# Performance work log

Hardware: AMD Instinct MI355X
Metric: run time of the kernel (lower is better)

The kernel has to match this reference:

```python
import jax, jax.numpy as jnp
import numpy as np

B, C, P, T, H = 4, 256, 1024, 64, 8
D = C // H
SCALE = float(np.sqrt(D * T))


def setup_inputs() -> dict:
    key = jax.random.key(0)
    ks = jax.random.split(key, 7)
    s = 1.0 / np.sqrt(C)
    return {
        "x": jax.random.normal(ks[0], (B, C, P, T), dtype=jnp.float32),
        "Wk": jax.random.uniform(ks[1], (C, C), dtype=jnp.float32, minval=-s, maxval=s),
        "bk": jax.random.uniform(ks[2], (C,), dtype=jnp.float32, minval=-s, maxval=s),
        "Wq": jax.random.uniform(ks[3], (C, C), dtype=jnp.float32, minval=-s, maxval=s),
        "bq": jax.random.uniform(ks[4], (C,), dtype=jnp.float32, minval=-s, maxval=s),
        "Wv": jax.random.uniform(ks[5], (C, C), dtype=jnp.float32, minval=-s, maxval=s),
        "bv": jax.random.uniform(ks[6], (C,), dtype=jnp.float32, minval=-s, maxval=s),
    }


def _proj_split(x, W, b):
    # 1x1 conv == channel-mixing linear; then split heads: b (h d) p t -> b h d p t
    y = jnp.einsum('bcpt,oc->bopt', x, W) + b[None, :, None, None]
    Bs, _, Ps, Ts = y.shape
    return y.reshape(Bs, H, D, Ps, Ts)


def reference(x, Wk, bk, Wq, bq, Wv, bv):
    k = _proj_split(x, Wk, bk)
    q = _proj_split(x, Wq, bq)
    v = _proj_split(x, Wv, bv)
    # contract jointly over d and t
    energy = jnp.einsum('bhdpt,bhdqt->bhpq', k, q)
    attn = jax.nn.softmax(energy / SCALE, axis=-1)
    out = jnp.einsum('bhpq,bhdpt->bhdqt', attn, v)
    # merge heads: b h d q t -> b (h d) q t
    return out.reshape(B, C, P, T)
```

## Files before the change

kernel.cpp:

```cpp
#include <hip/hip_runtime.h>
#include <cstdint>
#include <cstddef>

#define NB 4
#define NC 256
#define NP 1024
#define NT 64
#define NH 8
#define ND 32
#define NF 2048
#define NPT 65536
#define KQV_ELEMS 67108864ull
#define INV_SCALE 0.022097086912079608f
#define MHAT 4.0f

typedef unsigned short u16;
typedef __bf16 bf16x8 __attribute__((ext_vector_type(8)));
typedef short  s16x8  __attribute__((ext_vector_type(8)));
typedef short  s16x4  __attribute__((ext_vector_type(4)));
typedef float  f32x4  __attribute__((ext_vector_type(4)));

__device__ __forceinline__ u16 f2bf(float f) {
  unsigned u = __builtin_bit_cast(unsigned, f);
  u += 0x7fffu + ((u >> 16) & 1u);
  return (u16)(u >> 16);
}
__device__ __forceinline__ float bf2f(u16 h) {
  unsigned u = ((unsigned)h) << 16;
  return __builtin_bit_cast(float, u);
}
__device__ __forceinline__ int swz(int row) { return ((row ^ (row >> 3)) & 7) << 4; }

#define GLOAD_LDS16(gp, lp) __builtin_amdgcn_global_load_lds( \
    (const __attribute__((address_space(1))) void*)(gp),      \
    (__attribute__((address_space(3))) void*)(lp), 16, 0, 0)

__device__ __forceinline__ f32x4 mfma16(bf16x8 a, bf16x8 b, f32x4 c) {
  return __builtin_amdgcn_mfma_f32_16x16x32_bf16(a, b, c, 0, 0, 0);
}

__global__ __launch_bounds__(256) void wcast_kernel(
    const float* __restrict__ Wk, const float* __restrict__ Wq,
    const float* __restrict__ Wv, u16* __restrict__ wbf)
{
  int pj = blockIdx.y;
  const float* W = (pj == 0) ? Wk : ((pj == 1) ? Wq : Wv);
  int idx = blockIdx.x * 1024 + threadIdx.x * 4;
  float4 v = *(const float4*)(W + idx);
  s16x4 pk;
  pk[0] = (short)f2bf(v.x); pk[1] = (short)f2bf(v.y);
  pk[2] = (short)f2bf(v.z); pk[3] = (short)f2bf(v.w);
  *(s16x4*)(wbf + (size_t)pj * 65536 + idx) = pk;
}

__global__ __launch_bounds__(256, 2) void xcast_kernel(
    const float* __restrict__ x, u16* __restrict__ xT)
{
  int ptt = blockIdx.x;
  int ct  = blockIdx.y;
  int b   = blockIdx.z;
  __shared__ __align__(16) u16 L[64 * 64];
  int tid = threadIdx.x;
#pragma unroll
  for (int i = 0; i < 4; i++) {
    int cl  = i * 16 + (tid >> 4);
    int ptl = (tid & 15) * 4;
    float4 v = *(const float4*)(x + ((size_t)(b * NC + ct * 64 + cl)) * NPT +
                                ptt * 64 + ptl);
    s16x4 pk;
    pk[0] = (short)f2bf(v.x); pk[1] = (short)f2bf(v.y);
    pk[2] = (short)f2bf(v.z); pk[3] = (short)f2bf(v.w);
    *(s16x4*)((char*)L + ((cl * 128 + ptl * 2) ^ swz(cl))) = pk;
  }
  __syncthreads();
#pragma unroll
  for (int i = 0; i < 2; i++) {
    int ptl = i * 32 + (tid >> 3);
    int c8  = (tid & 7) * 8;
    s16x8 v;
#pragma unroll
    for (int j = 0; j < 8; j++) {
      int row = c8 + j;
      v[j] = (short)*(const u16*)((char*)L + ((row * 128 + ptl * 2) ^ swz(row)));
    }
    *(s16x8*)(xT + ((size_t)b * NPT + (size_t)ptt * 64 + ptl) * NC + ct * 64 + c8) = v;
  }
}

__global__ __launch_bounds__(256, 2) void transpose_kernel(
    const u16* __restrict__ in, u16* __restrict__ outp,
    const float* __restrict__ sscale)
{
  int ft = blockIdx.x;
  int pt = blockIdx.y;
  int slab = blockIdx.z;
  __shared__ __align__(16) u16 L[64 * 64];
  int t = threadIdx.x;
  const u16* ip = in + (size_t)slab * NP * NF;
#pragma unroll
  for (int i = 0; i < 2; i++) {
    int pl = i * 32 + (t >> 3);
    int c8 = (t & 7) * 8;
    s16x8 v = *(const s16x8*)(ip + (size_t)(pt * 64 + pl) * NF + ft * 64 + c8);
    *(s16x8*)((char*)L + ((pl * 128 + c8 * 2) ^ swz(pl))) = v;
  }
  __syncthreads();
  u16* op = outp + (size_t)slab * NP * NF;
#pragma unroll
  for (int i = 0; i < 2; i++) {
    int fl = i * 32 + (t >> 3);
    int p8 = (t & 7) * 8;
    const float* sc = sscale + slab * 1024 + pt * 64 + p8;
    s16x8 v;
#pragma unroll
    for (int j2 = 0; j2 < 8; j2++) {
      int row = p8 + j2;
      u16 raw = *(const u16*)((char*)L + ((row * 128 + fl * 2) ^ swz(row)));
      v[j2] = (short)f2bf(bf2f(raw) * sc[j2]);
    }
    *(s16x8*)(op + (size_t)(ft * 64 + fl) * NP + pt * 64 + p8) = v;
  }
}

#define PJSTG(TT) do {                                                         \
    GLOAD_LDS16(Ag + (size_t)psrow * NC + (TT) * 32 + psg * 8,                 \
                L + ((((TT) & 1) * 32768 + pdst) >> 1));                       \
    GLOAD_LDS16(Bg + (size_t)psrow * NC + (TT) * 32 + psg * 8,                 \
                L + ((((TT) & 1) * 32768 + 16384 + pdst) >> 1));               \
  } while (0)

#define PJBODY(J, WAITASM, DOSTG) do {                                         \
    if (DOSTG) PJSTG((J) + 1);                                                 \
    __builtin_amdgcn_sched_barrier(0);                                         \
    asm volatile(WAITASM ::: "memory");                                        \
    __builtin_amdgcn_s_barrier();                                              \
    __builtin_amdgcn_sched_barrier(0);                                         \
    {                                                                          \
      const int bb = ((J) & 1) * 32768;                                        \
      bf16x8 af[4], bfr[4];                                                    \
      _Pragma("unroll")                                                        \
      for (int mf = 0; mf < 4; mf++)                                           \
        af[mf] = *(const bf16x8*)((char*)L + bb + baseA + mf * 1024);          \
      _Pragma("unroll")                                                        \
      for (int nf = 0; nf < 4; nf++)                                           \
        bfr[nf] = *(const bf16x8*)((char*)L + bb + 16384 + baseB + nf * 1024); \
      __builtin_amdgcn_s_setprio(1);                                           \
      _Pragma("unroll")                                                        \
      for (int mf = 0; mf < 4; mf++)                                           \
        _Pragma("unroll")                                                      \
        for (int nf = 0; nf < 4; nf++)                                         \
          acc[mf][nf] = mfma16(af[mf], bfr[nf], acc[mf][nf]);                  \
      __builtin_amdgcn_s_setprio(0);                                           \
    }                                                                          \
    __builtin_amdgcn_sched_barrier(0);                                         \
    asm volatile("s_waitcnt lgkmcnt(0)" ::: "memory");                         \
    __builtin_amdgcn_s_barrier();                                              \
    asm volatile("" ::: "memory");                                             \
    __builtin_amdgcn_sched_barrier(0);                                         \
  } while (0)

__global__ __launch_bounds__(1024) void proj1024_kernel(
    const u16* __restrict__ wbf, const u16* __restrict__ xT,
    const float* __restrict__ bk, const float* __restrict__ bq,
    const float* __restrict__ bv, u16* __restrict__ kqv)
{
  __shared__ __align__(16) u16 L[32768];
  int d0 = blockIdx.x;
  int b  = blockIdx.y;
  int xcd = d0 & 7, r = d0 >> 3;
  int pj  = r % 3, tch = r / 3;
  int ptile = tch * 8 + xcd;
  const float* bias = (pj == 0) ? bk : ((pj == 1) ? bq : bv);
  u16* outb = kqv + (size_t)pj * KQV_ELEMS;
  const int n0 = ptile * 256;

  const u16* Ag = wbf + (size_t)pj * 65536;
  const u16* Bg = xT + ((size_t)b * NPT + (size_t)n0) * NC;

  const int tid  = threadIdx.x;
  const int lane = tid & 63;
  const int wv   = tid >> 6;
  const int wr = wv >> 2, wc = wv & 3;

  const int psrow = tid >> 2;
  const int psg   = (lane & 3) ^ ((lane >> 3) & 3);
  const int pdst  = wv * 1024;

  const int ra0 = wr * 64 + (lane & 15);
  const int rb0 = wc * 64 + (lane & 15);
  const int gk  = lane >> 4;
  const int baseA = ra0 * 64 + ((gk ^ ((ra0 >> 1) & 3)) << 4);
  const int baseB = rb0 * 64 + ((gk ^ ((rb0 >> 1) & 3)) << 4);

  f32x4 acc[4][4];
#pragma unroll
  for (int a = 0; a < 4; a++)
#pragma unroll
    for (int c = 0; c < 4; c++) acc[a][c] = (f32x4){0.f, 0.f, 0.f, 0.f};

  PJSTG(0);
  __builtin_amdgcn_sched_barrier(0);

  PJBODY(0, "s_waitcnt vmcnt(2)", 1);
  PJBODY(1, "s_waitcnt vmcnt(2)", 1);
  PJBODY(2, "s_waitcnt vmcnt(2)", 1);
  PJBODY(3, "s_waitcnt vmcnt(2)", 1);
  PJBODY(4, "s_waitcnt vmcnt(2)", 1);
  PJBODY(5, "s_waitcnt vmcnt(2)", 1);
  PJBODY(6, "s_waitcnt vmcnt(2)", 1);
  PJBODY(7, "s_waitcnt vmcnt(0)", 0);

#pragma unroll
  for (int mf = 0; mf < 4; mf++) {
#pragma unroll
    for (int jj = 0; jj < 4; jj++) {
      int o = wr * 64 + mf * 16 + (lane >> 4) * 4 + jj;
      float bsv = bias[o];
      int hh = o >> 5, dd = o & 31;
#pragma unroll
      for (int nf = 0; nf < 4; nf++) {
        int n = n0 + wc * 64 + nf * 16 + (lane & 15);
        int p = n >> 6, t = n & 63;
        outb[((size_t)(b * NH + hh) * NP + p) * NF + dd * 64 + t] =
            f2bf(acc[mf][nf][jj] + bsv);
      }
    }
  }
}

#define STG1(TT, I, OP) do {                                                   \
    const u16* gp_ = (OP ? Bg : Ag) + (size_t)grow[I] * KT + (TT) * 32 + gcol[I]; \
    GLOAD_LDS16(gp_, L + ((((TT) & 3) * 32768 + (OP) * 16384 +                 \
                           ((I) & 1 ? W1 : W0)) >> 1));                        \
  } while (0)

#define FENCE() do {                                                           \
    asm volatile("" ::: "memory");                                             \
    __builtin_amdgcn_sched_barrier(0);                                         \
  } while (0)

#define KBODY(J, WAITASM, DOSTG) do {                                          \
    const int bufb_ = ((J) & 3) * 32768;                                       \
    bf16x8 a_[4], b_[4];                                                       \
    _Pragma("unroll")                                                          \
    for (int mf = 0; mf < 4; mf++)                                             \
      a_[mf] = *(const bf16x8*)((const char*)L + bufb_ + baseA + mf * 1024);   \
    _Pragma("unroll")                                                          \
    for (int nf = 0; nf < 4; nf++)                                             \
      b_[nf] = *(const bf16x8*)((const char*)L + bufb_ + baseB + nf * 1024);   \
    if (DOSTG) { STG1((J) + 3, 0, 0); STG1((J) + 3, 1, 0); }                   \
    __builtin_amdgcn_s_barrier();                                              \
    asm volatile("s_waitcnt lgkmcnt(0)" ::: "memory");                         \
    __builtin_amdgcn_sched_barrier(0);                                         \
    __builtin_amdgcn_s_setprio(1);                                             \
    _Pragma("unroll")                                                          \
    for (int mf = 0; mf < 4; mf++)                                             \
      _Pragma("unroll")                                                        \
      for (int nf = 0; nf < 4; nf++)                                           \
        acc[mf][nf] = mfma16(a_[mf], b_[nf], acc[mf][nf]);                     \
    __builtin_amdgcn_s_setprio(0);                                             \
    __builtin_amdgcn_sched_barrier(0);                                         \
    __builtin_amdgcn_s_barrier();                                              \
    FENCE();                                                                   \
    bf16x8 a2_[4];                                                             \
    _Pragma("unroll")                                                          \
    for (int mf = 0; mf < 4; mf++)                                             \
      a2_[mf] = *(const bf16x8*)((const char*)L + bufb_ + baseA +              \
                                 (4 + mf) * 1024);                             \
    if (DOSTG) { STG1((J) + 3, 2, 1); STG1((J) + 3, 3, 1); }                   \
    __builtin_amdgcn_s_barrier();                                              \
    asm volatile("s_waitcnt lgkmcnt(0)" ::: "memory");                         \
    __builtin_amdgcn_sched_barrier(0);                                         \
    __builtin_amdgcn_s_setprio(1);                                             \
    _Pragma("unroll")                                                          \
    for (int mf = 0; mf < 4; mf++)                                             \
      _Pragma("unroll")                                                        \
      for (int nf = 0; nf < 4; nf++)                                           \
        acc[4 + mf][nf] = mfma16(a2_[mf], b_[nf], acc[4 + mf][nf]);            \
    __builtin_amdgcn_s_setprio(0);                                             \
    __builtin_amdgcn_sched_barrier(0);                                         \
    asm volatile(WAITASM ::: "memory");                                        \
    __builtin_amdgcn_s_barrier();                                              \
    FENCE();                                                                   \
  } while (0)

template <int KT>
__device__ __forceinline__ void core256(const u16* __restrict__ Ag,
                                        const u16* __restrict__ Bg,
                                        u16* L, f32x4 acc[8][4])
{
  constexpr int NKT = KT / 32;
  const int tid  = threadIdx.x;
  const int lane = tid & 63;
  const int wv   = tid >> 6;
  const int wr = wv >> 2, wc = wv & 3;

  int grow[4], gcol[4];
#pragma unroll
  for (int i = 0; i < 4; i++) {
    int oi   = (tid + (i & 1) * 512) * 16;
    int loff = oi ^ (((oi >> 7) & 3) << 4);
    grow[i] = loff >> 6;
    gcol[i] = (loff & 63) >> 1;
  }
  const int W0 = wv * 1024;
  const int W1 = wv * 1024 + 8192;

  const int rowA  = wr * 128 + (lane & 15);
  const int baseA = rowA * 64 + ((((lane >> 4)) ^ ((rowA >> 1) & 3)) << 4);
  const int rowB  = wc * 64 + (lane & 15);
  const int baseB = 16384 + rowB * 64 + ((((lane >> 4)) ^ ((rowB >> 1) & 3)) << 4);

#pragma unroll
  for (int tt = 0; tt < 3; tt++) {
    STG1(tt, 0, 0); STG1(tt, 1, 0); STG1(tt, 2, 1); STG1(tt, 3, 1);
  }
  __builtin_amdgcn_sched_barrier(0);
  asm volatile("s_waitcnt vmcnt(8)" ::: "memory");
  __builtin_amdgcn_s_barrier();
  FENCE();

  for (int j = 0; j < NKT - 3; ++j)
    KBODY(j, "s_waitcnt vmcnt(8)", 1);
  KBODY(NKT - 3, "s_waitcnt vmcnt(4)", 0);
  KBODY(NKT - 2, "s_waitcnt vmcnt(0)", 0);
  KBODY(NKT - 1, "", 0);
}

__global__ __launch_bounds__(512, 2) void qk256_kernel(
    const u16* __restrict__ kb, const u16* __restrict__ qb,
    u16* __restrict__ Pb, float* __restrict__ pstats)
{
  extern __shared__ u16 L[];
  int bid = blockIdx.x;
  int xcd = bid & 7, r = bid >> 3;
  int bh  = xcd * 4 + (r >> 4);
  int til = r & 15;
  int mt  = til >> 2, nt = til & 3;

  const u16* Ag = qb + (size_t)bh * NP * NF + (size_t)mt * 256 * NF;
  const u16* Bg = kb + (size_t)bh * NP * NF + (size_t)nt * 256 * NF;

  f32x4 acc[8][4];
#pragma unroll
  for (int a = 0; a < 8; a++)
#pragma unroll
    for (int c = 0; c < 4; c++) acc[a][c] = (f32x4){0.f, 0.f, 0.f, 0.f};

  core256<NF>(Ag, Bg, L, acc);

  const int tid  = threadIdx.x;
  const int lane = tid & 63, wv = tid >> 6;
  const int wr = wv >> 2, wc = wv & 3;
  u16* Pp = Pb + (size_t)bh * NP * NP;

  float l4[4] = {0.f, 0.f, 0.f, 0.f};
#pragma unroll
  for (int mf = 0; mf < 8; mf++)
#pragma unroll
    for (int jj = 0; jj < 4; jj++) {
      int m = mt * 256 + wr * 128 + mf * 16 + (lane >> 4) * 4 + jj;
#pragma unroll
      for (int nf = 0; nf < 4; nf++) {
        int n = nt * 256 + wc * 64 + nf * 16 + (lane & 15);
        float e = __expf(acc[mf][nf][jj] * INV_SCALE - MHAT);
        l4[nf] += e;
        Pp[(size_t)m * NP + n] = f2bf(e);
      }
    }

#pragma unroll
  for (int nf = 0; nf < 4; nf++) {
    l4[nf] += __shfl_xor(l4[nf], 16);
    l4[nf] += __shfl_xor(l4[nf], 32);
  }
  float* st = (float*)L;
  __syncthreads();
  if (lane < 16) {
#pragma unroll
    for (int nf = 0; nf < 4; nf++)
      st[wr * 256 + wc * 64 + nf * 16 + lane] = l4[nf];
  }
  __syncthreads();
  if (tid < 256) {
    float s = st[tid] + st[256 + tid];
    pstats[((bh * 4 + mt) << 10) + nt * 256 + tid] = s;
  }
}

__global__ __launch_bounds__(256) void statsfin_kernel(
    const float* __restrict__ pstats, float* __restrict__ sscale)
{
  int idx = blockIdx.x * 256 + threadIdx.x;
  int bh = idx >> 10, p = idx & 1023;
  const float* pp = pstats + (size_t)bh * 4096 + p;
  float s = pp[0] + pp[1024] + pp[2048] + pp[3072];
  sscale[idx] = 1.0f / s;
}

__global__ __launch_bounds__(512, 2) void av256_kernel(
    const u16* __restrict__ Pb, const u16* __restrict__ Vt, float* __restrict__ out)
{
  extern __shared__ u16 L[];
  int bid = blockIdx.x;
  int xcd = bid & 7, r = bid >> 3;
  int bh  = xcd * 4 + (r >> 5);
  int til = r & 31;
  int mt  = til >> 3, ntf = til & 7;

  const u16* Ag = Pb + (size_t)bh * NP * NP + (size_t)mt * 256 * NP;
  const u16* Bg = Vt + (size_t)bh * NF * NP + (size_t)ntf * 256 * NP;

  f32x4 acc[8][4];
#pragma unroll
  for (int a = 0; a < 8; a++)
#pragma unroll
    for (int c = 0; c < 4; c++) acc[a][c] = (f32x4){0.f, 0.f, 0.f, 0.f};

  core256<NP>(Ag, Bg, L, acc);

  const int lane = threadIdx.x & 63, wv = threadIdx.x >> 6;
  const int wr = wv >> 2, wc = wv & 3;
  int b = bh >> 3, h = bh & 7;
#pragma unroll
  for (int mf = 0; mf < 8; mf++)
#pragma unroll
    for (int jj = 0; jj < 4; jj++) {
      int m = mt * 256 + wr * 128 + mf * 16 + (lane >> 4) * 4 + jj;
#pragma unroll
      for (int nf = 0; nf < 4; nf++) {
        int n = ntf * 256 + wc * 64 + nf * 16 + (lane & 15);
        int dd = n >> 6, t = n & 63;
        out[((size_t)(b * NC + h * ND + dd) * NP + m) * NT + t] = acc[mf][nf][jj];
      }
    }
}

extern "C" void kernel_launch(void* const* d_in, const int* in_sizes, int n_in,
                              void* d_out, int out_size, void* d_ws, size_t ws_size,
                              hipStream_t stream)
{
  if (ws_size < 4ull * KQV_ELEMS * sizeof(u16)) return;

  const float* x  = (const float*)d_in[0];
  const float* Wk = (const float*)d_in[1];
  const float* bk = (const float*)d_in[2];
  const float* Wq = (const float*)d_in[3];
  const float* bq = (const float*)d_in[4];
  const float* Wv = (const float*)d_in[5];
  const float* bv = (const float*)d_in[6];

  u16* kb = (u16*)d_ws;
  u16* qb = kb + KQV_ELEMS;
  u16* vb = kb + 2 * KQV_ELEMS;
  u16* Pb = kb + 3 * KQV_ELEMS;
  float* pstats = (float*)(Pb + 33554432);
  float* sscale = pstats + 131072;
  u16* vt = kb;

  u16* xT  = (u16*)d_out;
  u16* wbf = xT + KQV_ELEMS;

  (void)hipFuncSetAttribute((const void*)qk256_kernel,
                            hipFuncAttributeMaxDynamicSharedMemorySize, 131072);
  (void)hipFuncSetAttribute((const void*)av256_kernel,
                            hipFuncAttributeMaxDynamicSharedMemorySize, 131072);

  wcast_kernel<<<dim3(64, 3), 256, 0, stream>>>(Wk, Wq, Wv, wbf);
  xcast_kernel<<<dim3(1024, 4, 4), 256, 0, stream>>>(x, xT);
  proj1024_kernel<<<dim3(768, 4), 1024, 0, stream>>>(wbf, xT, bk, bq, bv, kb);
  qk256_kernel<<<dim3(512), 512, 131072, stream>>>(kb, qb, Pb, pstats);
  statsfin_kernel<<<dim3(128), 256, 0, stream>>>(pstats, sscale);
  transpose_kernel<<<dim3(32, 16, 32), 256, 0, stream>>>(vb, vt, sscale);
  av256_kernel<<<dim3(1024), 512, 131072, stream>>>(Pb, vt, (float*)d_out);
}
```

Measured before the change: 636.4 us.

## Restructure GEMM main loop to triple-buffered single-phase stages and fuse stats finalize

The shared GEMM core moves from a 4-stage ring with two half-steps per K tile (separate A-half loads and barriers) to a 3-stage ring. Each iteration issues all four global-to-LDS loads for a tile two steps ahead, waits once, then runs all 32 MFMAs. This cuts LDS from 128KB to 96KB per block and halves the barrier count per tile. Separately, the statsfin kernel is removed and the transpose kernel computes the reciprocal row sums from pstats itself, saving one launch. The trade-off is a shallower prefetch distance, which may expose more memory latency, plus some redundant reciprocal work in the transpose.

```diff
diff --git a/kernel.cpp b/kernel.cpp
--- a/kernel.cpp
+++ b/kernel.cpp
@@ -89,7 +89,7 @@
 
 __global__ __launch_bounds__(256, 2) void transpose_kernel(
     const u16* __restrict__ in, u16* __restrict__ outp,
-    const float* __restrict__ sscale)
+    const float* __restrict__ pstats)
 {
   int ft = blockIdx.x;
   int pt = blockIdx.y;
@@ -105,12 +105,16 @@
     *(s16x8*)((char*)L + ((pl * 128 + c8 * 2) ^ swz(pl))) = v;
   }
   __syncthreads();
+  int p8 = (t & 7) * 8;
+  const float* pp = pstats + slab * 4096 + pt * 64 + p8;
+  float sc[8];
+#pragma unroll
+  for (int j2 = 0; j2 < 8; j2++)
+    sc[j2] = 1.0f / (pp[j2] + pp[j2 + 1024] + pp[j2 + 2048] + pp[j2 + 3072]);
   u16* op = outp + (size_t)slab * NP * NF;
 #pragma unroll
   for (int i = 0; i < 2; i++) {
     int fl = i * 32 + (t >> 3);
-    int p8 = (t & 7) * 8;
-    const float* sc = sscale + slab * 1024 + pt * 64 + p8;
     s16x8 v;
 #pragma unroll
     for (int j2 = 0; j2 < 8; j2++) {
@@ -228,60 +232,47 @@
   }
 }
 
-#define STG1(TT, I, OP) do {                                                   \
-    const u16* gp_ = (OP ? Bg : Ag) + (size_t)grow[I] * KT + (TT) * 32 + gcol[I]; \
-    GLOAD_LDS16(gp_, L + ((((TT) & 3) * 32768 + (OP) * 16384 +                 \
-                           ((I) & 1 ? W1 : W0)) >> 1));                        \
+#define STG2(BASE, TT) do {                                                    \
+    GLOAD_LDS16(Ag + (size_t)grow[0] * KT + (TT) * 32 + gcol[0],               \
+                L + (((BASE) + W0) >> 1));                                     \
+    GLOAD_LDS16(Ag + (size_t)grow[1] * KT + (TT) * 32 + gcol[1],               \
+                L + (((BASE) + W1) >> 1));                                     \
+    GLOAD_LDS16(Bg + (size_t)grow[2] * KT + (TT) * 32 + gcol[2],               \
+                L + (((BASE) + 16384 + W0) >> 1));                             \
+    GLOAD_LDS16(Bg + (size_t)grow[3] * KT + (TT) * 32 + gcol[3],               \
+                L + (((BASE) + 16384 + W1) >> 1));                             \
   } while (0)
 
-#define FENCE() do {                                                           \
-    asm volatile("" ::: "memory");                                             \
-    __builtin_amdgcn_sched_barrier(0);                                         \
-  } while (0)
-
-#define KBODY(J, WAITASM, DOSTG) do {                                          \
-    const int bufb_ = ((J) & 3) * 32768;                                       \
-    bf16x8 a_[4], b_[4];                                                       \
-    _Pragma("unroll")                                                          \
-    for (int mf = 0; mf < 4; mf++)                                             \
-      a_[mf] = *(const bf16x8*)((const char*)L + bufb_ + baseA + mf * 1024);   \
-    _Pragma("unroll")                                                          \
-    for (int nf = 0; nf < 4; nf++)                                             \
-      b_[nf] = *(const bf16x8*)((const char*)L + bufb_ + baseB + nf * 1024);   \
-    if (DOSTG) { STG1((J) + 3, 0, 0); STG1((J) + 3, 1, 0); }                   \
-    __builtin_amdgcn_s_barrier();                                              \
-    asm volatile("s_waitcnt lgkmcnt(0)" ::: "memory");                         \
-    __builtin_amdgcn_sched_barrier(0);                                         \
-    __builtin_amdgcn_s_setprio(1);                                             \
-    _Pragma("unroll")                                                          \
-    for (int mf = 0; mf < 4; mf++)                                             \
-      _Pragma("unroll")                                                        \
-      for (int nf = 0; nf < 4; nf++)                                           \
-        acc[mf][nf] = mfma16(a_[mf], b_[nf], acc[mf][nf]);                     \
-    __builtin_amdgcn_s_setprio(0);                                             \
-    __builtin_amdgcn_sched_barrier(0);                                         \
-    __builtin_amdgcn_s_barrier();                                              \
-    FENCE();                                                                   \
-    bf16x8 a2_[4];                                                             \
-    _Pragma("unroll")                                                          \
-    for (int mf = 0; mf < 4; mf++)                                             \
-      a2_[mf] = *(const bf16x8*)((const char*)L + bufb_ + baseA +              \
-                                 (4 + mf) * 1024);                             \
-    if (DOSTG) { STG1((J) + 3, 2, 1); STG1((J) + 3, 3, 1); }                   \
-    __builtin_amdgcn_s_barrier();                                              \
-    asm volatile("s_waitcnt lgkmcnt(0)" ::: "memory");                         \
-    __builtin_amdgcn_sched_barrier(0);                                         \
-    __builtin_amdgcn_s_setprio(1);                                             \
-    _Pragma("unroll")                                                          \
-    for (int mf = 0; mf < 4; mf++)                                             \
-      _Pragma("unroll")                                                        \
-      for (int nf = 0; nf < 4; nf++)                                           \
-        acc[4 + mf][nf] = mfma16(a2_[mf], b_[nf], acc[4 + mf][nf]);            \
-    __builtin_amdgcn_s_setprio(0);                                             \
+#define KBODY2(CB, WAITASM, DOSTG, SB, TT) do {                                \
+    if (DOSTG) STG2((SB) * 32768, TT);                                         \
     __builtin_amdgcn_sched_barrier(0);                                         \
     asm volatile(WAITASM ::: "memory");                                        \
     __builtin_amdgcn_s_barrier();                                              \
-    FENCE();                                                                   \
+    __builtin_amdgcn_sched_barrier(0);                                         \
+    {                                                                          \
+      const int bb = (CB) * 32768;                                             \
+      bf16x8 a_[8], b_[4];                                                     \
+      _Pragma("unroll")                                                        \
+      for (int mf = 0; mf < 8; mf++)                                           \
+        a_[mf] = *(const bf16x8*)((const char*)L + bb + baseA + mf * 1024);    \
+      _Pragma("unroll")                                                        \
+      for (int nf = 0; nf < 4; nf++)                                           \
+        b_[nf] = *(const bf16x8*)((const char*)L + bb + 16384 + baseB +        \
+                                  nf * 1024);                                  \
+      asm volatile("s_waitcnt lgkmcnt(0)" ::: "memory");                       \
+      __builtin_amdgcn_sched_barrier(0);                                       \
+      __builtin_amdgcn_s_setprio(1);                                           \
+      _Pragma("unroll")                                                        \
+      for (int mf = 0; mf < 8; mf++)                                           \
+        _Pragma("unroll")                                                      \
+        for (int nf = 0; nf < 4; nf++)                                         \
+          acc[mf][nf] = mfma16(a_[mf], b_[nf], acc[mf][nf]);                   \
+      __builtin_amdgcn_s_setprio(0);                                           \
+    }                                                                          \
+    __builtin_amdgcn_sched_barrier(0);                                         \
+    __builtin_amdgcn_s_barrier();                                              \
+    asm volatile("" ::: "memory");                                             \
+    __builtin_amdgcn_sched_barrier(0);                                         \
   } while (0)
 
 template <int KT>
@@ -309,22 +300,21 @@
   const int rowA  = wr * 128 + (lane & 15);
   const int baseA = rowA * 64 + ((((lane >> 4)) ^ ((rowA >> 1) & 3)) << 4);
   const int rowB  = wc * 64 + (lane & 15);
-  const int baseB = 16384 + rowB * 64 + ((((lane >> 4)) ^ ((rowB >> 1) & 3)) << 4);
-
-#pragma unroll
-  for (int tt = 0; tt < 3; tt++) {
-    STG1(tt, 0, 0); STG1(tt, 1, 0); STG1(tt, 2, 1); STG1(tt, 3, 1);
-  }
+  const int baseB = rowB * 64 + ((((lane >> 4)) ^ ((rowB >> 1) & 3)) << 4);
+
+  STG2(0, 0);
+  STG2(32768, 1);
   __builtin_amdgcn_sched_barrier(0);
-  asm volatile("s_waitcnt vmcnt(8)" ::: "memory");
-  __builtin_amdgcn_s_barrier();
-  FENCE();
-
-  for (int j = 0; j < NKT - 3; ++j)
-    KBODY(j, "s_waitcnt vmcnt(8)", 1);
-  KBODY(NKT - 3, "s_waitcnt vmcnt(4)", 0);
-  KBODY(NKT - 2, "s_waitcnt vmcnt(0)", 0);
-  KBODY(NKT - 1, "", 0);
+
+  int cb = 0, sb = 2;
+  for (int j = 0; j < NKT - 2; ++j) {
+    KBODY2(cb, "s_waitcnt vmcnt(8)", 1, sb, j + 2);
+    cb = (cb == 2) ? 0 : cb + 1;
+    sb = (sb == 2) ? 0 : sb + 1;
+  }
+  KBODY2(cb, "s_waitcnt vmcnt(4)", 0, 0, 0);
+  cb = (cb == 2) ? 0 : cb + 1;
+  KBODY2(cb, "s_waitcnt vmcnt(0)", 0, 0, 0);
 }
 
 __global__ __launch_bounds__(512, 2) void qk256_kernel(
@@ -388,16 +378,6 @@
   }
 }
 
-__global__ __launch_bounds__(256) void statsfin_kernel(
-    const float* __restrict__ pstats, float* __restrict__ sscale)
-{
-  int idx = blockIdx.x * 256 + threadIdx.x;
-  int bh = idx >> 10, p = idx & 1023;
-  const float* pp = pstats + (size_t)bh * 4096 + p;
-  float s = pp[0] + pp[1024] + pp[2048] + pp[3072];
-  sscale[idx] = 1.0f / s;
-}
-
 __global__ __launch_bounds__(512, 2) void av256_kernel(
     const u16* __restrict__ Pb, const u16* __restrict__ Vt, float* __restrict__ out)
 {
@@ -455,22 +435,20 @@
   u16* vb = kb + 2 * KQV_ELEMS;
   u16* Pb = kb + 3 * KQV_ELEMS;
   float* pstats = (float*)(Pb + 33554432);
-  float* sscale = pstats + 131072;
   u16* vt = kb;
 
   u16* xT  = (u16*)d_out;
   u16* wbf = xT + KQV_ELEMS;
 
   (void)hipFuncSetAttribute((const void*)qk256_kernel,
-                            hipFuncAttributeMaxDynamicSharedMemorySize, 131072);
+                            hipFuncAttributeMaxDynamicSharedMemorySize, 98304);
   (void)hipFuncSetAttribute((const void*)av256_kernel,
-                            hipFuncAttributeMaxDynamicSharedMemorySize, 131072);
+                            hipFuncAttributeMaxDynamicSharedMemorySize, 98304);
 
   wcast_kernel<<<dim3(64, 3), 256, 0, stream>>>(Wk, Wq, Wv, wbf);
   xcast_kernel<<<dim3(1024, 4, 4), 256, 0, stream>>>(x, xT);
   proj1024_kernel<<<dim3(768, 4), 1024, 0, stream>>>(wbf, xT, bk, bq, bv, kb);
-  qk256_kernel<<<dim3(512), 512, 131072, stream>>>(kb, qb, Pb, pstats);
-  statsfin_kernel<<<dim3(128), 256, 0, stream>>>(pstats, sscale);
-  transpose_kernel<<<dim3(32, 16, 32), 256, 0, stream>>>(vb, vt, sscale);
-  av256_kernel<<<dim3(1024), 512, 131072, stream>>>(Pb, vt, (float*)d_out);
-}
+  qk256_kernel<<<dim3(512), 512, 98304, stream>>>(kb, qb, Pb, pstats);
+  transpose_kernel<<<dim3(32, 16, 32), 256, 0, stream>>>(vb, vt, pstats);
+  av256_kernel<<<dim3(1024), 512, 98304, stream>>>(Pb, vt, (float*)d_out);
+}
```

Result: slower. 661.2 us (+3.9%).

## Fuse softmax-sum finalize into V transpose and cut barriers in MFMA loop

Applied to the files above, without the earlier changes.

Removes the separate statsfin kernel: the transpose kernel now sums the four partial row sums and takes the reciprocal itself, saving one launch and one small buffer round trip. The shared GEMM core loop now issues all LDS fragment loads and global-to-LDS staging for an iteration at once. It keeps only the trailing barrier and uses a partial lgkmcnt wait so the first MFMA group can start earlier. This trades fewer barrier stalls for higher register pressure and tighter reliance on the buffer rotation for LDS hazard safety.

```diff
diff --git a/kernel.cpp b/kernel.cpp
--- a/kernel.cpp
+++ b/kernel.cpp
@@ -89,7 +89,7 @@
 
 __global__ __launch_bounds__(256, 2) void transpose_kernel(
     const u16* __restrict__ in, u16* __restrict__ outp,
-    const float* __restrict__ sscale)
+    const float* __restrict__ pstats)
 {
   int ft = blockIdx.x;
   int pt = blockIdx.y;
@@ -105,12 +105,16 @@
     *(s16x8*)((char*)L + ((pl * 128 + c8 * 2) ^ swz(pl))) = v;
   }
   __syncthreads();
+  int p8 = (t & 7) * 8;
+  const float* pp = pstats + slab * 4096 + pt * 64 + p8;
+  float sc[8];
+#pragma unroll
+  for (int j2 = 0; j2 < 8; j2++)
+    sc[j2] = 1.0f / (pp[j2] + pp[j2 + 1024] + pp[j2 + 2048] + pp[j2 + 3072]);
   u16* op = outp + (size_t)slab * NP * NF;
 #pragma unroll
   for (int i = 0; i < 2; i++) {
     int fl = i * 32 + (t >> 3);
-    int p8 = (t & 7) * 8;
-    const float* sc = sscale + slab * 1024 + pt * 64 + p8;
     s16x8 v;
 #pragma unroll
     for (int j2 = 0; j2 < 8; j2++) {
@@ -239,18 +243,24 @@
     __builtin_amdgcn_sched_barrier(0);                                         \
   } while (0)
 
-#define KBODY(J, WAITASM, DOSTG) do {                                          \
+#define KBODY3(J, WAITASM, DOSTG) do {                                         \
     const int bufb_ = ((J) & 3) * 32768;                                       \
-    bf16x8 a_[4], b_[4];                                                       \
+    bf16x8 a_[4], b_[4], a2_[4];                                               \
     _Pragma("unroll")                                                          \
     for (int mf = 0; mf < 4; mf++)                                             \
       a_[mf] = *(const bf16x8*)((const char*)L + bufb_ + baseA + mf * 1024);   \
     _Pragma("unroll")                                                          \
     for (int nf = 0; nf < 4; nf++)                                             \
       b_[nf] = *(const bf16x8*)((const char*)L + bufb_ + baseB + nf * 1024);   \
-    if (DOSTG) { STG1((J) + 3, 0, 0); STG1((J) + 3, 1, 0); }                   \
-    __builtin_amdgcn_s_barrier();                                              \
-    asm volatile("s_waitcnt lgkmcnt(0)" ::: "memory");                         \
+    __builtin_amdgcn_sched_barrier(0);  \
+    _Pragma("unroll")                                                          \
+    for (int mf = 0; mf < 4; mf++)                                             \
+      a2_[mf] = *(const bf16x8*)((const char*)L + bufb_ + baseA +              \
+                                 (4 + mf) * 1024);                             \
+    if (DOSTG) { STG1((J) + 3, 0, 0); STG1((J) + 3, 1, 0);                     \
+                 STG1((J) + 3, 2, 1); STG1((J) + 3, 3, 1); }                   \
+    __builtin_amdgcn_sched_barrier(0);                                         \
+    asm volatile("s_waitcnt lgkmcnt(4)" ::: "memory");       \
     __builtin_amdgcn_sched_barrier(0);                                         \
     __builtin_amdgcn_s_setprio(1);                                             \
     _Pragma("unroll")                                                          \
@@ -260,16 +270,7 @@
         acc[mf][nf] = mfma16(a_[mf], b_[nf], acc[mf][nf]);                     \
     __builtin_amdgcn_s_setprio(0);                                             \
     __builtin_amdgcn_sched_barrier(0);                                         \
-    __builtin_amdgcn_s_barrier();                                              \
-    FENCE();                                                                   \
-    bf16x8 a2_[4];                                                             \
-    _Pragma("unroll")                                                          \
-    for (int mf = 0; mf < 4; mf++)                                             \
-      a2_[mf] = *(const bf16x8*)((const char*)L + bufb_ + baseA +              \
-                                 (4 + mf) * 1024);                             \
-    if (DOSTG) { STG1((J) + 3, 2, 1); STG1((J) + 3, 3, 1); }                   \
-    __builtin_amdgcn_s_barrier();                                              \
-    asm volatile("s_waitcnt lgkmcnt(0)" ::: "memory");                         \
+    asm volatile("s_waitcnt lgkmcnt(0)" ::: "memory");   \
     __builtin_amdgcn_sched_barrier(0);                                         \
     __builtin_amdgcn_s_setprio(1);                                             \
     _Pragma("unroll")                                                          \
@@ -321,10 +322,10 @@
   FENCE();
 
   for (int j = 0; j < NKT - 3; ++j)
-    KBODY(j, "s_waitcnt vmcnt(8)", 1);
-  KBODY(NKT - 3, "s_waitcnt vmcnt(4)", 0);
-  KBODY(NKT - 2, "s_waitcnt vmcnt(0)", 0);
-  KBODY(NKT - 1, "", 0);
+    KBODY3(j, "s_waitcnt vmcnt(8)", 1);
+  KBODY3(NKT - 3, "s_waitcnt vmcnt(4)", 0);
+  KBODY3(NKT - 2, "s_waitcnt vmcnt(0)", 0);
+  KBODY3(NKT - 1, "", 0);
 }
 
 __global__ __launch_bounds__(512, 2) void qk256_kernel(
@@ -388,16 +389,6 @@
   }
 }
 
-__global__ __launch_bounds__(256) void statsfin_kernel(
-    const float* __restrict__ pstats, float* __restrict__ sscale)
-{
-  int idx = blockIdx.x * 256 + threadIdx.x;
-  int bh = idx >> 10, p = idx & 1023;
-  const float* pp = pstats + (size_t)bh * 4096 + p;
-  float s = pp[0] + pp[1024] + pp[2048] + pp[3072];
-  sscale[idx] = 1.0f / s;
-}
-
 __global__ __launch_bounds__(512, 2) void av256_kernel(
     const u16* __restrict__ Pb, const u16* __restrict__ Vt, float* __restrict__ out)
 {
@@ -455,7 +446,6 @@
   u16* vb = kb + 2 * KQV_ELEMS;
   u16* Pb = kb + 3 * KQV_ELEMS;
   float* pstats = (float*)(Pb + 33554432);
-  float* sscale = pstats + 131072;
   u16* vt = kb;
 
   u16* xT  = (u16*)d_out;
@@ -470,7 +460,6 @@
   xcast_kernel<<<dim3(1024, 4, 4), 256, 0, stream>>>(x, xT);
   proj1024_kernel<<<dim3(768, 4), 1024, 0, stream>>>(wbf, xT, bk, bq, bv, kb);
   qk256_kernel<<<dim3(512), 512, 131072, stream>>>(kb, qb, Pb, pstats);
-  statsfin_kernel<<<dim3(128), 256, 0, stream>>>(pstats, sscale);
-  transpose_kernel<<<dim3(32, 16, 32), 256, 0, stream>>>(vb, vt, sscale);
+  transpose_kernel<<<dim3(32, 16, 32), 256, 0, stream>>>(vb, vt, pstats);
   av256_kernel<<<dim3(1024), 512, 131072, stream>>>(Pb, vt, (float*)d_out);
 }
```

Measured after the change: 638.4 us. Within noise of the previous version (+0.3%).
